# Kernel optimization log

Hardware: AMD Instinct MI355X
Metric: run time of the kernel (lower is better)

The kernel has to match this reference:

```python
import jax, jax.numpy as jnp
import numpy as np

N = 8192
D_IN = 512
D_OUT = 64
ALPHA = 0.2  # LeakyReLU negative slope
MASK_VAL = -9e15


def setup_inputs() -> dict:
    key = jax.random.key(0)
    k1, k2, k3, k4 = jax.random.split(key, 4)
    inp = jax.random.normal(k1, (N, D_IN), dtype=jnp.float32)
    adj = (jax.random.uniform(k2, (N, N)) < 0.05).astype(jnp.float32)
    adj = adj.at[jnp.arange(N), jnp.arange(N)].set(1.0)
    W = jax.random.normal(k3, (D_IN, D_OUT), dtype=jnp.float32) * 0.05
    a = jax.random.normal(k4, (2 * D_OUT, 1), dtype=jnp.float32) * 0.05
    return {"input": inp, "adj": adj, "W": W, "a": a}


def reference(input, adj, W, a):
    # h = input @ W : [n, out]
    h = input @ W
    # Algebraic equivalent of the dense pairwise concat:
    # e_ij = leakyrelu([h_i || h_j] . a) = leakyrelu(h_i.a1 + h_j.a2)
    a1, a2 = a[:D_OUT, 0], a[D_OUT:, 0]          # [out], [out]
    e = jax.nn.leaky_relu(
        (h @ a1)[:, None] + (h @ a2)[None, :],    # [n, n]
        negative_slope=ALPHA,
    )
    attention = jnp.where(adj > 0, e, MASK_VAL)
    attention = jax.nn.softmax(attention, axis=1)
    out = attention @ h                            # [n, out]
    return jax.nn.elu(out)                         # end=False branch
```

## Files before the change

### kernel.cpp

```cpp
#include <hip/hip_runtime.h>
#include <hip/hip_bf16.h>

#define N 8192
#define D_IN 512
#define D_OUT 64
#define ALPHA 0.2f
#define BM 16
#define BK 128
#define NSTEP (N / BK)

typedef __attribute__((ext_vector_type(4))) float f32x4;
typedef __attribute__((ext_vector_type(8))) short bf16x8;

static __device__ __forceinline__ unsigned pk_bf16(float lo, float hi) {
    unsigned ulo = __bfloat16_as_ushort(__float2bfloat16(lo));
    unsigned uhi = __bfloat16_as_ushort(__float2bfloat16(hi));
    return (uhi << 16) | ulo;
}

#define BARRIER() do { \
    asm volatile("s_waitcnt lgkmcnt(0)" ::: "memory"); \
    __builtin_amdgcn_sched_barrier(0); \
    __builtin_amdgcn_s_barrier(); \
    __builtin_amdgcn_sched_barrier(0); \
} while (0)

__global__ __launch_bounds__(256) void gat_h_kernel(
    const float* __restrict__ input, const float* __restrict__ W,
    const float* __restrict__ a, unsigned short* __restrict__ hbT,
    float* __restrict__ s1, float* __restrict__ s2)
{
    int wave = (blockIdx.x * 256 + threadIdx.x) >> 6;
    int lane = threadIdx.x & 63;
    int row0 = wave * 4;
    const float* in0 = input + (size_t)row0 * D_IN;
    float a1 = a[lane], a2 = a[D_OUT + lane];
    float acc[4];
#pragma unroll
    for (int r = 0; r < 4; ++r) acc[r] = 0.f;
#pragma unroll 4
    for (int k = 0; k < D_IN; ++k) {
        float wk = W[k * D_OUT + lane];
#pragma unroll
        for (int r = 0; r < 4; ++r)
            acc[r] = fmaf(in0[(size_t)r * D_IN + k], wk, acc[r]);
    }
    uint2 hv;
    hv.x = pk_bf16(acc[0], acc[1]);
    hv.y = pk_bf16(acc[2], acc[3]);
    *(uint2*)(hbT + (size_t)lane * N + row0) = hv;
#pragma unroll
    for (int r = 0; r < 4; ++r) {
        float p1 = acc[r] * a1;
        float p2 = acc[r] * a2;
#pragma unroll
        for (int off = 32; off; off >>= 1) {
            p1 += __shfl_xor(p1, off, 64);
            p2 += __shfl_xor(p2, off, 64);
        }
        if (lane == 0) { s1[row0 + r] = p1; s2[row0 + r] = p2; }
    }
}

struct Pref { float4 a0, a1, s0, s1; uint4 h0, h1, h2, h3; };

static __device__ __forceinline__ void issue(Pref& p, const float* ab,
                                             const float* sb,
                                             const unsigned short* hb, int j0) {
    p.a0 = *(const float4*)(ab + j0);
    p.a1 = *(const float4*)(ab + j0 + 4);
    p.s0 = *(const float4*)(sb + j0);
    p.s1 = *(const float4*)(sb + j0 + 4);
    p.h0 = *(const uint4*)(hb + j0);
    p.h1 = *(const uint4*)(hb + j0 + 8);
    p.h2 = *(const uint4*)(hb + j0 + 16);
    p.h3 = *(const uint4*)(hb + j0 + 24);
}

__global__ __launch_bounds__(256, 3) void gat_flash_kernel(
    const float* __restrict__ adj, const unsigned short* __restrict__ hbT,
    const float* __restrict__ s1, const float* __restrict__ s2,
    float* __restrict__ out)
{
    __shared__ __align__(16) unsigned char Pl[2][BM * BK * 2];
    __shared__ __align__(16) unsigned char Hl[2][D_OUT * BK * 2];
    __shared__ float lsl[BM];

    const int tid  = threadIdx.x;
    const int lane = tid & 63;
    const int wv   = tid >> 6;
    const int r    = tid >> 4;
    const int s    = tid & 15;
    const int hd   = tid >> 2;
    const int hc   = tid & 3;
    const int rg   = blockIdx.x * BM + r;

    const float* adj_base = adj + (size_t)rg * N + s * 8;
    const float* s2_base  = s2 + s * 8;
    const unsigned short* hb_base = hbT + (size_t)hd * N + hc * 32;
    float s1r = s1[rg];
    float eref = s1r + s2[rg];
    eref = eref > 0.f ? eref : ALPHA * eref;
    float lsum = 0.f;
    f32x4 acc = {0.f, 0.f, 0.f, 0.f};

    auto stage = [&](const Pref& p, int b) {
        const float* av0 = (const float*)&p.a0;
        const float* av1 = (const float*)&p.a1;
        const float* sv0 = (const float*)&p.s0;
        const float* sv1 = (const float*)&p.s1;
        float w[8];
#pragma unroll
        for (int z = 0; z < 4; ++z) {
            float e0 = s1r + sv0[z]; e0 = e0 > 0.f ? e0 : ALPHA * e0;
            float e1 = s1r + sv1[z]; e1 = e1 > 0.f ? e1 : ALPHA * e1;
            float w0 = __expf(e0 - eref);
            float w1 = __expf(e1 - eref);
            w[z]     = av0[z] > 0.f ? w0 : 0.f;
            w[z + 4] = av1[z] > 0.f ? w1 : 0.f;
        }
#pragma unroll
        for (int z = 0; z < 8; ++z) lsum += w[z];
        uint4 pk;
        pk.x = pk_bf16(w[0], w[1]); pk.y = pk_bf16(w[2], w[3]);
        pk.z = pk_bf16(w[4], w[5]); pk.w = pk_bf16(w[6], w[7]);
        *(uint4*)(&Pl[b][r * 256 + ((s * 16) ^ ((r & 7) << 4))]) = pk;
        *(uint4*)(&Hl[b][hd * 256 + ((hc * 64 +  0) ^ ((hd & 7) << 4))]) = p.h0;
        *(uint4*)(&Hl[b][hd * 256 + ((hc * 64 + 16) ^ ((hd & 7) << 4))]) = p.h1;
        *(uint4*)(&Hl[b][hd * 256 + ((hc * 64 + 32) ^ ((hd & 7) << 4))]) = p.h2;
        *(uint4*)(&Hl[b][hd * 256 + ((hc * 64 + 48) ^ ((hd & 7) << 4))]) = p.h3;
    };

    auto mfma_step = [&](int c) {
        const unsigned char* Pc = Pl[c];
        const unsigned char* Hc = Hl[c];
        const int i  = lane & 15;
        const int kb = lane >> 4;
        const int dd = wv * 16 + (lane & 15);
#pragma unroll
        for (int kk = 0; kk < 4; ++kk) {
            uint4 ua = *(const uint4*)(Pc + i * 256 + ((kk * 64 + kb * 16) ^ ((i & 7) << 4)));
            uint4 ub = *(const uint4*)(Hc + dd * 256 + ((kk * 64 + kb * 16) ^ ((dd & 7) << 4)));
            acc = __builtin_amdgcn_mfma_f32_16x16x32_bf16(
                __builtin_bit_cast(bf16x8, ua), __builtin_bit_cast(bf16x8, ub), acc, 0, 0, 0);
        }
    };

    Pref RA, RB;
    issue(RA, adj_base, s2_base, hb_base, 0);
    issue(RB, adj_base, s2_base, hb_base, BK);
    stage(RA, 0);
    issue(RA, adj_base, s2_base, hb_base, 2 * BK);
    BARRIER();

    for (int ks = 0; ks < NSTEP; ks += 2) {
        mfma_step(0);
        stage(RB, 1);
        if (ks + 3 < NSTEP) issue(RB, adj_base, s2_base, hb_base, (ks + 3) * BK);
        BARRIER();
        mfma_step(1);
        if (ks + 2 < NSTEP) {
            stage(RA, 0);
            if (ks + 4 < NSTEP) issue(RA, adj_base, s2_base, hb_base, (ks + 4) * BK);
        }
        BARRIER();
    }

#pragma unroll
    for (int off = 8; off; off >>= 1) lsum += __shfl_xor(lsum, off, 64);
    if ((tid & 15) == 0) lsl[r] = lsum;
    __syncthreads();

    const int dd = wv * 16 + (lane & 15);
#pragma unroll
    for (int reg = 0; reg < 4; ++reg) {
        int i = (lane >> 4) * 4 + reg;
        float o = acc[reg] / lsl[i];
        o = o > 0.f ? o : expm1f(o);
        out[(size_t)(blockIdx.x * BM + i) * 64 + dd] = o;
    }
}

extern "C" void kernel_launch(void* const* d_in, const int* in_sizes, int n_in,
                              void* d_out, int out_size, void* d_ws, size_t ws_size,
                              hipStream_t stream) {
    const float* input = (const float*)d_in[0];
    const float* adj   = (const float*)d_in[1];
    const float* W     = (const float*)d_in[2];
    const float* a     = (const float*)d_in[3];
    float* out = (float*)d_out;

    unsigned short* hbT = (unsigned short*)d_ws;
    float* s1 = (float*)(hbT + (size_t)N * D_OUT);
    float* s2 = s1 + N;

    gat_h_kernel<<<512, 256, 0, stream>>>(input, W, a, hbT, s1, s2);
    gat_flash_kernel<<<N / BM, 256, 0, stream>>>(adj, hbT, s1, s2, out);
}
```

Baseline: 120.0 us.

## Split neighbor dimension across two blocks and load pre-packed H fragments directly

The h matrix is written in an MFMA-fragment-packed layout so each wave loads its B operands straight from global memory into registers, which removes the H staging through LDS. The N dimension is split in half across blocks (split-K, 1024 blocks instead of 512). A new reduce kernel sums the partial accumulators and softmax denominators, then applies ELU. Occupancy hint rises to 4 blocks per CU. The cost is an extra kernel launch and a partial-sum round trip through global memory.

```diff
diff --git a/kernel.cpp b/kernel.cpp
--- a/kernel.cpp
+++ b/kernel.cpp
@@ -7,7 +7,7 @@
 #define ALPHA 0.2f
 #define BM 16
 #define BK 128
-#define NSTEP (N / BK)
+#define NSH 32
 
 typedef __attribute__((ext_vector_type(4))) float f32x4;
 typedef __attribute__((ext_vector_type(8))) short bf16x8;
@@ -27,7 +27,7 @@
 
 __global__ __launch_bounds__(256) void gat_h_kernel(
     const float* __restrict__ input, const float* __restrict__ W,
-    const float* __restrict__ a, unsigned short* __restrict__ hbT,
+    const float* __restrict__ a, unsigned short* __restrict__ hpk,
     float* __restrict__ s1, float* __restrict__ s2)
 {
     int wave = (blockIdx.x * 256 + threadIdx.x) >> 6;
@@ -45,10 +45,15 @@
         for (int r = 0; r < 4; ++r)
             acc[r] = fmaf(in0[(size_t)r * D_IN + k], wk, acc[r]);
     }
-    uint2 hv;
-    hv.x = pk_bf16(acc[0], acc[1]);
-    hv.y = pk_bf16(acc[2], acc[3]);
-    *(uint2*)(hbT + (size_t)lane * N + row0) = hv;
+    {
+        int ks = row0 >> 7, kk = (row0 >> 5) & 3, kb = (row0 >> 3) & 3, eo = row0 & 7;
+        int wvd = lane >> 4, dd = lane & 15;
+        size_t off = ((size_t)(((ks * 4 + wvd) * 4 + kk) * 64) + kb * 16 + dd) * 8 + eo;
+        uint2 hv;
+        hv.x = pk_bf16(acc[0], acc[1]);
+        hv.y = pk_bf16(acc[2], acc[3]);
+        *(uint2*)(hpk + off) = hv;
+    }
 #pragma unroll
     for (int r = 0; r < 4; ++r) {
         float p1 = acc[r] * a1;
@@ -62,49 +67,51 @@
     }
 }
 
-struct Pref { float4 a0, a1, s0, s1; uint4 h0, h1, h2, h3; };
-
-static __device__ __forceinline__ void issue(Pref& p, const float* ab,
-                                             const float* sb,
-                                             const unsigned short* hb, int j0) {
+struct ASP { float4 a0, a1, s0, s1; };
+struct UBP { uint4 b0, b1, b2, b3; };
+
+static __device__ __forceinline__ void issue_as(ASP& p, const float* ab,
+                                                const float* sb, int j0) {
     p.a0 = *(const float4*)(ab + j0);
     p.a1 = *(const float4*)(ab + j0 + 4);
     p.s0 = *(const float4*)(sb + j0);
     p.s1 = *(const float4*)(sb + j0 + 4);
-    p.h0 = *(const uint4*)(hb + j0);
-    p.h1 = *(const uint4*)(hb + j0 + 8);
-    p.h2 = *(const uint4*)(hb + j0 + 16);
-    p.h3 = *(const uint4*)(hb + j0 + 24);
-}
-
-__global__ __launch_bounds__(256, 3) void gat_flash_kernel(
-    const float* __restrict__ adj, const unsigned short* __restrict__ hbT,
+}
+static __device__ __forceinline__ void issue_ub(UBP& p, const unsigned short* hb,
+                                                int ksg) {
+    const unsigned short* f = hb + ((size_t)ksg << 13);
+    p.b0 = *(const uint4*)(f);
+    p.b1 = *(const uint4*)(f + 512);
+    p.b2 = *(const uint4*)(f + 1024);
+    p.b3 = *(const uint4*)(f + 1536);
+}
+
+__global__ __launch_bounds__(256, 4) void gat_flash_kernel(
+    const float* __restrict__ adj, const unsigned short* __restrict__ hpk,
     const float* __restrict__ s1, const float* __restrict__ s2,
-    float* __restrict__ out)
+    float* __restrict__ pacc, float* __restrict__ plsum)
 {
     __shared__ __align__(16) unsigned char Pl[2][BM * BK * 2];
-    __shared__ __align__(16) unsigned char Hl[2][D_OUT * BK * 2];
-    __shared__ float lsl[BM];
 
     const int tid  = threadIdx.x;
     const int lane = tid & 63;
     const int wv   = tid >> 6;
     const int r    = tid >> 4;
     const int s    = tid & 15;
-    const int hd   = tid >> 2;
-    const int hc   = tid & 3;
-    const int rg   = blockIdx.x * BM + r;
-
-    const float* adj_base = adj + (size_t)rg * N + s * 8;
-    const float* s2_base  = s2 + s * 8;
-    const unsigned short* hb_base = hbT + (size_t)hd * N + hc * 32;
+    const int hf   = blockIdx.x >> 9;
+    const int rb   = blockIdx.x & 511;
+    const int rg   = rb * BM + r;
+
+    const float* adj_base = adj + (size_t)rg * N + hf * 4096 + s * 8;
+    const float* s2_base  = s2 + hf * 4096 + s * 8;
+    const unsigned short* hb_base = hpk + ((size_t)hf * NSH << 13) + (wv << 11) + (lane << 3);
     float s1r = s1[rg];
     float eref = s1r + s2[rg];
     eref = eref > 0.f ? eref : ALPHA * eref;
     float lsum = 0.f;
     f32x4 acc = {0.f, 0.f, 0.f, 0.f};
 
-    auto stage = [&](const Pref& p, int b) {
+    auto stage = [&](const ASP& p, int b) {
         const float* av0 = (const float*)&p.a0;
         const float* av1 = (const float*)&p.a1;
         const float* sv0 = (const float*)&p.s0;
@@ -125,60 +132,69 @@
         pk.x = pk_bf16(w[0], w[1]); pk.y = pk_bf16(w[2], w[3]);
         pk.z = pk_bf16(w[4], w[5]); pk.w = pk_bf16(w[6], w[7]);
         *(uint4*)(&Pl[b][r * 256 + ((s * 16) ^ ((r & 7) << 4))]) = pk;
-        *(uint4*)(&Hl[b][hd * 256 + ((hc * 64 +  0) ^ ((hd & 7) << 4))]) = p.h0;
-        *(uint4*)(&Hl[b][hd * 256 + ((hc * 64 + 16) ^ ((hd & 7) << 4))]) = p.h1;
-        *(uint4*)(&Hl[b][hd * 256 + ((hc * 64 + 32) ^ ((hd & 7) << 4))]) = p.h2;
-        *(uint4*)(&Hl[b][hd * 256 + ((hc * 64 + 48) ^ ((hd & 7) << 4))]) = p.h3;
     };
 
-    auto mfma_step = [&](int c) {
+    auto mfma_step = [&](int c, const UBP& u) {
         const unsigned char* Pc = Pl[c];
-        const unsigned char* Hc = Hl[c];
         const int i  = lane & 15;
         const int kb = lane >> 4;
-        const int dd = wv * 16 + (lane & 15);
+        const uint4 ub[4] = {u.b0, u.b1, u.b2, u.b3};
 #pragma unroll
         for (int kk = 0; kk < 4; ++kk) {
             uint4 ua = *(const uint4*)(Pc + i * 256 + ((kk * 64 + kb * 16) ^ ((i & 7) << 4)));
-            uint4 ub = *(const uint4*)(Hc + dd * 256 + ((kk * 64 + kb * 16) ^ ((dd & 7) << 4)));
             acc = __builtin_amdgcn_mfma_f32_16x16x32_bf16(
-                __builtin_bit_cast(bf16x8, ua), __builtin_bit_cast(bf16x8, ub), acc, 0, 0, 0);
+                __builtin_bit_cast(bf16x8, ua), __builtin_bit_cast(bf16x8, ub[kk]),
+                acc, 0, 0, 0);
         }
     };
 
-    Pref RA, RB;
-    issue(RA, adj_base, s2_base, hb_base, 0);
-    issue(RB, adj_base, s2_base, hb_base, BK);
-    stage(RA, 0);
-    issue(RA, adj_base, s2_base, hb_base, 2 * BK);
+    ASP AS_A, AS_B;
+    UBP U_A, U_B;
+    issue_as(AS_A, adj_base, s2_base, 0);
+    issue_as(AS_B, adj_base, s2_base, BK);
+    issue_ub(U_A, hb_base, 0);
+    issue_ub(U_B, hb_base, 1);
+    stage(AS_A, 0);
+    issue_as(AS_A, adj_base, s2_base, 2 * BK);
     BARRIER();
 
-    for (int ks = 0; ks < NSTEP; ks += 2) {
-        mfma_step(0);
-        stage(RB, 1);
-        if (ks + 3 < NSTEP) issue(RB, adj_base, s2_base, hb_base, (ks + 3) * BK);
+    for (int p = 0; p < NSH; p += 2) {
+        mfma_step(0, U_A);
+        if (p + 2 < NSH) issue_ub(U_A, hb_base, p + 2);
+        stage(AS_B, 1);
+        if (p + 3 < NSH) issue_as(AS_B, adj_base, s2_base, (p + 3) * BK);
         BARRIER();
-        mfma_step(1);
-        if (ks + 2 < NSTEP) {
-            stage(RA, 0);
-            if (ks + 4 < NSTEP) issue(RA, adj_base, s2_base, hb_base, (ks + 4) * BK);
+        mfma_step(1, U_B);
+        if (p + 3 < NSH) issue_ub(U_B, hb_base, p + 3);
+        if (p + 2 < NSH) {
+            stage(AS_A, 0);
+            if (p + 4 < NSH) issue_as(AS_A, adj_base, s2_base, (p + 4) * BK);
         }
         BARRIER();
     }
 
 #pragma unroll
     for (int off = 8; off; off >>= 1) lsum += __shfl_xor(lsum, off, 64);
-    if ((tid & 15) == 0) lsl[r] = lsum;
-    __syncthreads();
+    if ((tid & 15) == 0) plsum[hf * N + rg] = lsum;
 
     const int dd = wv * 16 + (lane & 15);
 #pragma unroll
     for (int reg = 0; reg < 4; ++reg) {
         int i = (lane >> 4) * 4 + reg;
-        float o = acc[reg] / lsl[i];
-        o = o > 0.f ? o : expm1f(o);
-        out[(size_t)(blockIdx.x * BM + i) * 64 + dd] = o;
-    }
+        pacc[((size_t)hf * N + rb * BM + i) * 64 + dd] = acc[reg];
+    }
+}
+
+__global__ __launch_bounds__(256) void gat_reduce_kernel(
+    const float* __restrict__ pacc, const float* __restrict__ plsum,
+    float* __restrict__ out)
+{
+    int idx = blockIdx.x * 256 + threadIdx.x;
+    int row = idx >> 6;
+    float aa = pacc[idx] + pacc[(size_t)N * 64 + idx];
+    float l  = plsum[row] + plsum[N + row];
+    float o  = aa / l;
+    out[idx] = o > 0.f ? o : expm1f(o);
 }
 
 extern "C" void kernel_launch(void* const* d_in, const int* in_sizes, int n_in,
@@ -190,10 +206,13 @@
     const float* a     = (const float*)d_in[3];
     float* out = (float*)d_out;
 
-    unsigned short* hbT = (unsigned short*)d_ws;
-    float* s1 = (float*)(hbT + (size_t)N * D_OUT);
-    float* s2 = s1 + N;
-
-    gat_h_kernel<<<512, 256, 0, stream>>>(input, W, a, hbT, s1, s2);
-    gat_flash_kernel<<<N / BM, 256, 0, stream>>>(adj, hbT, s1, s2, out);
-}
+    unsigned short* hpk = (unsigned short*)d_ws;
+    float* s1    = (float*)(hpk + (size_t)N * D_OUT);
+    float* s2    = s1 + N;
+    float* pacc  = s2 + N;
+    float* plsum = pacc + (size_t)2 * N * 64;
+
+    gat_h_kernel<<<512, 256, 0, stream>>>(input, W, a, hpk, s1, s2);
+    gat_flash_kernel<<<1024, 256, 0, stream>>>(adj, hpk, s1, s2, pacc, plsum);
+    gat_reduce_kernel<<<N * 64 / 256, 256, 0, stream>>>(pacc, plsum, out);
+}
```

After: 114.9 us. 4.2% less time.
